# Optimization experiments

Hardware: AMD Instinct MI355X
Metric: run time of the kernel (lower is better)

## Reference

```python
import jax, jax.numpy as jnp
import numpy as np

I, T, L, E, H, W = 256, 256, 32, 128, 7, 7

def setup_inputs() -> dict:
    key = jax.random.key(0)
    k1, k2, k3 = jax.random.split(key, 3)
    image_features = jax.random.normal(k1, (I, E, H, W), dtype=jnp.float32)
    text_features = jax.random.normal(k2, (T, L, E), dtype=jnp.float32)
    text_length = jax.random.randint(k3, (T,), 1, L + 1, dtype=jnp.int32)
    logit_neg_log_temperature = jnp.asarray(-np.log(0.07), dtype=jnp.float32)
    return {
        "image_features": image_features,
        "text_features": text_features,
        "text_length": text_length,
        "logit_neg_log_temperature": logit_neg_log_temperature,
    }

def reference(image_features, text_features, text_length, logit_neg_log_temperature):
    # image_features: [I, E, H, W]; text_features: [T, L, E]
    i, e, h, w = image_features.shape
    img = image_features.reshape(i, e, h * w)            # [I, E, HW]
    # cross-modal similarity per (image, text, token, patch): [I, T, L, HW]
    sim = jnp.einsum('iep,tle->itlp', img, text_features)
    # max over patches, then sum over tokens, normalized by caption length
    match_max = jnp.max(sim, axis=3)                     # [I, T, L]
    match = jnp.sum(match_max, axis=2) / text_length.astype(match_max.dtype)  # [I, T]
    logit_scale = jnp.exp(logit_neg_log_temperature)
    logits_per_image = match * logit_scale
    logits_per_text = match.T * logit_scale
    return (logits_per_image, logits_per_text)
```

## Files before the change

### kernel.cpp

```cpp
#include <hip/hip_runtime.h>
#include <hip/hip_bf16.h>

typedef __attribute__((ext_vector_type(8)))  short bf16x8;
typedef __attribute__((ext_vector_type(16))) float f32x16;

#define I_N 256
#define T_N 256
#define L_N 32
#define E_N 128
#define P_N 49

__global__ __launch_bounds__(256) void pack_all(const float* __restrict__ txt,
                                                const float* __restrict__ img,
                                                unsigned short* __restrict__ bpre,
                                                unsigned short* __restrict__ apre) {
    const int bid = blockIdx.x;
    if (bid < 512) {
        int gid  = bid * 256 + threadIdx.x;
        int lane = gid & 63;
        int ks   = (gid >> 6) & 7;
        int t    = gid >> 9;
        int l    = lane & 31;
        int e0   = ks * 16 + (lane >> 5) * 8;
        const float* src = txt + (t * L_N + l) * E_N + e0;
        union { unsigned short u[8]; bf16x8 v; } o;
        #pragma unroll
        for (int j = 0; j < 8; ++j) {
            __hip_bfloat16 h = __float2bfloat16(src[j]);
            o.u[j] = *reinterpret_cast<unsigned short*>(&h);
        }
        ((bf16x8*)bpre)[gid] = o.v;
    } else {
        int gid   = (bid - 512) * 256 + threadIdx.x;
        int lane  = gid & 63;
        int ks    = (gid >> 6) & 7;
        int pt    = (gid >> 9) & 1;
        int i     = gid >> 10;
        int patch = pt * 32 + (lane & 31);
        int e0    = ks * 16 + (lane >> 5) * 8;
        const float* src = img + i * (E_N * P_N) + e0 * P_N + patch;
        union { unsigned short u[8]; bf16x8 v; } o;
        #pragma unroll
        for (int j = 0; j < 8; ++j) {
            float x = (patch < P_N) ? src[j * P_N] : 0.0f;
            __hip_bfloat16 h = __float2bfloat16(x);
            o.u[j] = *reinterpret_cast<unsigned short*>(&h);
        }
        ((bf16x8*)apre)[gid] = o.v;
    }
}

__global__ __launch_bounds__(256, 3) void clip_mfma(
    const unsigned short* __restrict__ apre,
    const unsigned short* __restrict__ bpre,
    const int*   __restrict__ tlen,
    const float* __restrict__ nlt,
    float*       __restrict__ out) {

    const int wid  = threadIdx.x >> 6;
    const int lane = threadIdx.x & 63;
    const int b    = blockIdx.x;
    const int r    = b % 12;
    const int i    = (b / 12) * 4 + wid;
    const float scale = expf(nlt[0]);
    const bool  lo32  = (lane < 32);

    bf16x8 af[2][8];
    const bf16x8* ap = (const bf16x8*)apre + (size_t)i * 16 * 64;
    #pragma unroll
    for (int pt = 0; pt < 2; ++pt)
        #pragma unroll
        for (int ks = 0; ks < 8; ++ks)
            af[pt][ks] = ap[(pt * 8 + ks) * 64 + lane];

    const bf16x8* bp = (const bf16x8*)bpre;

    #pragma unroll 1
    for (int t = r; t < T_N; t += 12) {
        bf16x8 bf[8];
        const bf16x8* tb = bp + (size_t)t * 8 * 64;
        #pragma unroll
        for (int ks = 0; ks < 8; ++ks)
            bf[ks] = tb[ks * 64 + lane];

        f32x16 a0, a1;
        #pragma unroll
        for (int rr = 0; rr < 16; ++rr) { a0[rr] = 0.0f; a1[rr] = 0.0f; }

        __builtin_amdgcn_s_setprio(1);
        #pragma unroll
        for (int ks = 0; ks < 8; ++ks) {
            a0 = __builtin_amdgcn_mfma_f32_32x32x16_bf16(af[0][ks], bf[ks], a0, 0, 0, 0);
            a1 = __builtin_amdgcn_mfma_f32_32x32x16_bf16(af[1][ks], bf[ks], a1, 0, 0, 0);
        }
        __builtin_amdgcn_s_setprio(0);

        float m = a0[0];
        #pragma unroll
        for (int rr = 1; rr < 16; ++rr) m = fmaxf(m, a0[rr]);
        #pragma unroll
        for (int rr = 0; rr < 8; ++rr)  m = fmaxf(m, a1[rr]);
        m = fmaxf(m, lo32 ? a1[8] : -INFINITY);
        m = fmaxf(m, __shfl_xor(m, 32));
        float s = m;
        #pragma unroll
        for (int off = 1; off <= 16; off <<= 1)
            s += __shfl_xor(s, off);

        if (lane == 0) {
            float match = (s / (float)tlen[t]) * scale;
            out[i * T_N + t]             = match;
            out[I_N * T_N + t * I_N + i] = match;
        }
    }
}

extern "C" void kernel_launch(void* const* d_in, const int* in_sizes, int n_in,
                              void* d_out, int out_size, void* d_ws, size_t ws_size,
                              hipStream_t stream) {
    const float* img  = (const float*)d_in[0];
    const float* txt  = (const float*)d_in[1];
    const int*   tlen = (const int*)d_in[2];
    const float* nlt  = (const float*)d_in[3];
    float*       out  = (float*)d_out;

    unsigned short* bpre = (unsigned short*)d_ws;
    unsigned short* apre = (unsigned short*)((char*)d_ws + (2u << 20));

    pack_all<<<1536, 256, 0, stream>>>(txt, img, bpre, apre);

    clip_mfma<<<768, 256, 0, stream>>>(apre, bpre, tlen, nlt, out);
}
```

Baseline: 47.89 us.

## Double-buffer text tiles in MFMA loop and move token reduction to separate kernel

The MFMA kernel now prefetches the next text tile's B fragments into a second register buffer while it computes the current one, and reduces the per-lane patch maxima with a tree instead of a serial chain. It no longer does the cross-lane token sum and scaling. Instead it writes 64 per-lane maxima per (image, text) pair to workspace, and a new reduce kernel sums them, divides by caption length and writes both outputs. The goal is to hide B-load latency and shorten the dependent chain in the hot loop. In exchange it adds a 16 MB workspace write and read, an extra launch, lower occupancy from the launch bound of 2, and some redundant tiles when the stride does not divide evenly.

Measured after the change: 60.27 us. 25.9% more time.

```diff
diff --git a/kernel.cpp b/kernel.cpp
--- a/kernel.cpp
+++ b/kernel.cpp
@@ -50,20 +50,17 @@
     }
 }
 
-__global__ __launch_bounds__(256, 3) void clip_mfma(
+__global__ __launch_bounds__(256, 2) void clip_mfma(
     const unsigned short* __restrict__ apre,
     const unsigned short* __restrict__ bpre,
-    const int*   __restrict__ tlen,
-    const float* __restrict__ nlt,
-    float*       __restrict__ out) {
+    float* __restrict__ mws) {
 
     const int wid  = threadIdx.x >> 6;
     const int lane = threadIdx.x & 63;
     const int b    = blockIdx.x;
     const int r    = b % 12;
     const int i    = (b / 12) * 4 + wid;
-    const float scale = expf(nlt[0]);
-    const bool  lo32  = (lane < 32);
+    const bool lo32 = (lane < 32);
 
     bf16x8 af[2][8];
     const bf16x8* ap = (const bf16x8*)apre + (size_t)i * 16 * 64;
@@ -75,18 +72,16 @@
 
     const bf16x8* bp = (const bf16x8*)bpre;
 
-    #pragma unroll 1
-    for (int t = r; t < T_N; t += 12) {
-        bf16x8 bf[8];
+    auto loadB = [&](bf16x8 (&bf)[8], int t) {
         const bf16x8* tb = bp + (size_t)t * 8 * 64;
         #pragma unroll
         for (int ks = 0; ks < 8; ++ks)
             bf[ks] = tb[ks * 64 + lane];
+    };
 
-        f32x16 a0, a1;
+    auto mfmaT = [&](f32x16& a0, f32x16& a1, bf16x8 (&bf)[8]) {
         #pragma unroll
         for (int rr = 0; rr < 16; ++rr) { a0[rr] = 0.0f; a1[rr] = 0.0f; }
-
         __builtin_amdgcn_s_setprio(1);
         #pragma unroll
         for (int ks = 0; ks < 8; ++ks) {
@@ -94,24 +89,62 @@
             a1 = __builtin_amdgcn_mfma_f32_32x32x16_bf16(af[1][ks], bf[ks], a1, 0, 0, 0);
         }
         __builtin_amdgcn_s_setprio(0);
+    };
 
-        float m = a0[0];
+    auto treeStore = [&](f32x16& a0, f32x16& a1, int t) {
+        float x[8];
         #pragma unroll
-        for (int rr = 1; rr < 16; ++rr) m = fmaxf(m, a0[rr]);
+        for (int q = 0; q < 8; ++q) x[q] = fmaxf(a0[2 * q], a0[2 * q + 1]);
         #pragma unroll
-        for (int rr = 0; rr < 8; ++rr)  m = fmaxf(m, a1[rr]);
-        m = fmaxf(m, lo32 ? a1[8] : -INFINITY);
-        m = fmaxf(m, __shfl_xor(m, 32));
-        float s = m;
+        for (int q = 0; q < 4; ++q) x[q] = fmaxf(x[q], x[q + 4]);
+        float ma0 = fmaxf(fmaxf(x[0], x[1]), fmaxf(x[2], x[3]));
+        float y[4];
         #pragma unroll
-        for (int off = 1; off <= 16; off <<= 1)
-            s += __shfl_xor(s, off);
+        for (int q = 0; q < 4; ++q) y[q] = fmaxf(a1[2 * q], a1[2 * q + 1]);
+        float ma1 = fmaxf(fmaxf(y[0], y[1]), fmaxf(y[2], y[3]));
+        float m = fmaxf(ma0, ma1);
+        if (lo32) m = fmaxf(m, a1[8]);
+        mws[((size_t)i * T_N + t) * 64 + lane] = m;
+    };
 
-        if (lane == 0) {
-            float match = (s / (float)tlen[t]) * scale;
-            out[i * T_N + t]             = match;
-            out[I_N * T_N + t * I_N + i] = match;
-        }
+    bf16x8 bfA[8], bfB[8];
+    f32x16 aA0, aA1, aB0, aB1;
+
+    loadB(bfA, r);
+    #pragma unroll 1
+    for (int k = 0; k < 22; k += 2) {
+        int t0v = r + 12 * k;
+        int t1v = r + 12 * (k + 1); if (t1v >= T_N) t1v -= 12;
+        loadB(bfB, t1v);
+        mfmaT(aA0, aA1, bfA);
+        treeStore(aA0, aA1, t0v);
+        if (k + 2 < 22) loadB(bfA, r + 12 * (k + 2));
+        mfmaT(aB0, aB1, bfB);
+        treeStore(aB0, aB1, t1v);
+    }
+}
+
+__global__ __launch_bounds__(256) void reduce_k(
+    const float* __restrict__ mws,
+    const int*   __restrict__ tlen,
+    const float* __restrict__ nlt,
+    float*       __restrict__ out) {
+    const int wid  = threadIdx.x >> 6;
+    const int lane = threadIdx.x & 63;
+    const int pair = blockIdx.x * 4 + wid;
+    const int i = pair >> 8, t = pair & 255;
+
+    float v = mws[(size_t)pair * 64 + lane];
+    v = fmaxf(v, __shfl_xor(v, 32));
+    float s = v;
+    #pragma unroll
+    for (int off = 1; off <= 16; off <<= 1)
+        s += __shfl_xor(s, off);
+
+    if (lane == 0) {
+        float match = (s / (float)tlen[t]) * expf(nlt[0]);
+        out[i * T_N + t]             = match;
+        out[I_N * T_N + t * I_N + i] = match;
     }
 }
 
@@ -126,8 +159,9 @@
 
     unsigned short* bpre = (unsigned short*)d_ws;
     unsigned short* apre = (unsigned short*)((char*)d_ws + (2u << 20));
+    float*          mws  = (float*)((char*)d_ws + (6u << 20));
 
     pack_all<<<1536, 256, 0, stream>>>(txt, img, bpre, apre);
-
-    clip_mfma<<<768, 256, 0, stream>>>(apre, bpre, tlen, nlt, out);
+    clip_mfma<<<768, 256, 0, stream>>>(apre, bpre, mws);
+    reduce_k<<<16384, 256, 0, stream>>>(mws, tlen, nlt, out);
 }
```

## Register-block two images per wave and tile text range per block

Applied to the files above, without the earlier changes.

Each wave now keeps A fragments for two images in registers, so every loaded text tile feeds four MFMA chains instead of two. This halves the B-operand global/L2 traffic per MFMA and adds independent accumulators for more instruction-level parallelism. Blocks now cover a contiguous range of 16 texts and 8 images, giving 512 blocks instead of 768, with launch bounds lowered to 2 blocks per CU to make room for the extra registers. The setprio hints are removed. The cost is higher register pressure and lower occupancy, plus a coarser grid.

Result: faster. 45.87 us (-4.2%).

```diff
diff --git a/kernel.cpp b/kernel.cpp
--- a/kernel.cpp
+++ b/kernel.cpp
@@ -50,67 +50,77 @@
     }
 }
 
-__global__ __launch_bounds__(256, 3) void clip_mfma(
+__global__ __launch_bounds__(256, 2) void clip_mfma(
     const unsigned short* __restrict__ apre,
     const unsigned short* __restrict__ bpre,
     const int*   __restrict__ tlen,
     const float* __restrict__ nlt,
     float*       __restrict__ out) {
 
-    const int wid  = threadIdx.x >> 6;
-    const int lane = threadIdx.x & 63;
-    const int b    = blockIdx.x;
-    const int r    = b % 12;
-    const int i    = (b / 12) * 4 + wid;
+    const int wid   = threadIdx.x >> 6;
+    const int lane  = threadIdx.x & 63;
+    const int b     = blockIdx.x;
+    const int tbase = (b >> 5) << 4;
+    const int i0    = (b & 31) * 8 + wid * 2;
     const float scale = expf(nlt[0]);
     const bool  lo32  = (lane < 32);
 
-    bf16x8 af[2][8];
-    const bf16x8* ap = (const bf16x8*)apre + (size_t)i * 16 * 64;
+    bf16x8 af[2][2][8];
     #pragma unroll
-    for (int pt = 0; pt < 2; ++pt)
+    for (int im = 0; im < 2; ++im) {
+        const bf16x8* ap = (const bf16x8*)apre + (size_t)(i0 + im) * 16 * 64;
         #pragma unroll
-        for (int ks = 0; ks < 8; ++ks)
-            af[pt][ks] = ap[(pt * 8 + ks) * 64 + lane];
+        for (int pt = 0; pt < 2; ++pt)
+            #pragma unroll
+            for (int ks = 0; ks < 8; ++ks)
+                af[im][pt][ks] = ap[(pt * 8 + ks) * 64 + lane];
+    }
 
     const bf16x8* bp = (const bf16x8*)bpre;
 
     #pragma unroll 1
-    for (int t = r; t < T_N; t += 12) {
+    for (int t = tbase; t < tbase + 16; ++t) {
         bf16x8 bf[8];
         const bf16x8* tb = bp + (size_t)t * 8 * 64;
         #pragma unroll
         for (int ks = 0; ks < 8; ++ks)
             bf[ks] = tb[ks * 64 + lane];
 
-        f32x16 a0, a1;
+        f32x16 a00, a01, a10, a11;
         #pragma unroll
-        for (int rr = 0; rr < 16; ++rr) { a0[rr] = 0.0f; a1[rr] = 0.0f; }
+        for (int rr = 0; rr < 16; ++rr) {
+            a00[rr] = 0.0f; a01[rr] = 0.0f; a10[rr] = 0.0f; a11[rr] = 0.0f;
+        }
 
-        __builtin_amdgcn_s_setprio(1);
         #pragma unroll
         for (int ks = 0; ks < 8; ++ks) {
-            a0 = __builtin_amdgcn_mfma_f32_32x32x16_bf16(af[0][ks], bf[ks], a0, 0, 0, 0);
-            a1 = __builtin_amdgcn_mfma_f32_32x32x16_bf16(af[1][ks], bf[ks], a1, 0, 0, 0);
+            a00 = __builtin_amdgcn_mfma_f32_32x32x16_bf16(af[0][0][ks], bf[ks], a00, 0, 0, 0);
+            a01 = __builtin_amdgcn_mfma_f32_32x32x16_bf16(af[0][1][ks], bf[ks], a01, 0, 0, 0);
+            a10 = __builtin_amdgcn_mfma_f32_32x32x16_bf16(af[1][0][ks], bf[ks], a10, 0, 0, 0);
+            a11 = __builtin_amdgcn_mfma_f32_32x32x16_bf16(af[1][1][ks], bf[ks], a11, 0, 0, 0);
         }
-        __builtin_amdgcn_s_setprio(0);
 
-        float m = a0[0];
         #pragma unroll
-        for (int rr = 1; rr < 16; ++rr) m = fmaxf(m, a0[rr]);
-        #pragma unroll
-        for (int rr = 0; rr < 8; ++rr)  m = fmaxf(m, a1[rr]);
-        m = fmaxf(m, lo32 ? a1[8] : -INFINITY);
-        m = fmaxf(m, __shfl_xor(m, 32));
-        float s = m;
-        #pragma unroll
-        for (int off = 1; off <= 16; off <<= 1)
-            s += __shfl_xor(s, off);
-
-        if (lane == 0) {
-            float match = (s / (float)tlen[t]) * scale;
-            out[i * T_N + t]             = match;
-            out[I_N * T_N + t * I_N + i] = match;
+        for (int im = 0; im < 2; ++im) {
+            const f32x16& c0 = im ? a10 : a00;
+            const f32x16& c1 = im ? a11 : a01;
+            float m = c0[0];
+            #pragma unroll
+            for (int rr = 1; rr < 16; ++rr) m = fmaxf(m, c0[rr]);
+            #pragma unroll
+            for (int rr = 0; rr < 8; ++rr)  m = fmaxf(m, c1[rr]);
+            m = fmaxf(m, lo32 ? c1[8] : -INFINITY);
+            m = fmaxf(m, __shfl_xor(m, 32));
+            float s = m;
+            #pragma unroll
+            for (int off = 1; off <= 16; off <<= 1)
+                s += __shfl_xor(s, off);
+            if (lane == 0) {
+                float match = (s / (float)tlen[t]) * scale;
+                const int i = i0 + im;
+                out[i * T_N + t]             = match;
+                out[I_N * T_N + t * I_N + i] = match;
+            }
         }
     }
 }
@@ -128,6 +138,5 @@
     unsigned short* apre = (unsigned short*)((char*)d_ws + (2u << 20));
 
     pack_all<<<1536, 256, 0, stream>>>(txt, img, bpre, apre);
-
-    clip_mfma<<<768, 256, 0, stream>>>(apre, bpre, tlen, nlt, out);
+    clip_mfma<<<512, 256, 0, stream>>>(apre, bpre, tlen, nlt, out);
 }
```

## Double-buffer text tiles with register prefetch and rebalance grid to 512 blocks

Applied to the files above, without the earlier changes.

The MFMA kernel now gives each block a contiguous run of 32 texts instead of a stride-12 set, and launches 512 blocks instead of 768. It keeps two register buffers of B fragments so the load for the next text is issued while the current one's MFMAs and max/sum reduction run. The occupancy hint drops from 3 to 2 blocks per SIMD group to make room for the extra registers. The s_setprio hints are removed. The trade-off is lower occupancy and fewer blocks, in exchange for explicit latency hiding and even work per block (32 texts each versus uneven 21/22).

Result: slower. 53.23 us (+11.2%).

```diff
diff --git a/kernel.cpp b/kernel.cpp
--- a/kernel.cpp
+++ b/kernel.cpp
@@ -50,7 +50,7 @@
     }
 }
 
-__global__ __launch_bounds__(256, 3) void clip_mfma(
+__global__ __launch_bounds__(256, 2) void clip_mfma(
     const unsigned short* __restrict__ apre,
     const unsigned short* __restrict__ bpre,
     const int*   __restrict__ tlen,
@@ -60,8 +60,8 @@
     const int wid  = threadIdx.x >> 6;
     const int lane = threadIdx.x & 63;
     const int b    = blockIdx.x;
-    const int r    = b % 12;
-    const int i    = (b / 12) * 4 + wid;
+    const int t0   = (b & 7) * 32;
+    const int i    = (b >> 3) * 4 + wid;
     const float scale = expf(nlt[0]);
     const bool  lo32  = (lane < 32);
 
@@ -75,43 +75,56 @@
 
     const bf16x8* bp = (const bf16x8*)bpre;
 
-    #pragma unroll 1
-    for (int t = r; t < T_N; t += 12) {
-        bf16x8 bf[8];
+    auto loadB = [&](bf16x8 (&bf)[8], int t) {
         const bf16x8* tb = bp + (size_t)t * 8 * 64;
         #pragma unroll
         for (int ks = 0; ks < 8; ++ks)
             bf[ks] = tb[ks * 64 + lane];
+    };
 
-        f32x16 a0, a1;
+    auto mfmaT = [&](f32x16& a0, f32x16& a1, bf16x8 (&bf)[8]) {
         #pragma unroll
         for (int rr = 0; rr < 16; ++rr) { a0[rr] = 0.0f; a1[rr] = 0.0f; }
-
-        __builtin_amdgcn_s_setprio(1);
         #pragma unroll
         for (int ks = 0; ks < 8; ++ks) {
             a0 = __builtin_amdgcn_mfma_f32_32x32x16_bf16(af[0][ks], bf[ks], a0, 0, 0, 0);
             a1 = __builtin_amdgcn_mfma_f32_32x32x16_bf16(af[1][ks], bf[ks], a1, 0, 0, 0);
         }
-        __builtin_amdgcn_s_setprio(0);
+    };
 
-        float m = a0[0];
+    auto reduceT = [&](f32x16& c0, f32x16& c1, int t) {
+        float m = c0[0];
         #pragma unroll
-        for (int rr = 1; rr < 16; ++rr) m = fmaxf(m, a0[rr]);
+        for (int rr = 1; rr < 16; ++rr) m = fmaxf(m, c0[rr]);
         #pragma unroll
-        for (int rr = 0; rr < 8; ++rr)  m = fmaxf(m, a1[rr]);
-        m = fmaxf(m, lo32 ? a1[8] : -INFINITY);
+        for (int rr = 0; rr < 8; ++rr)  m = fmaxf(m, c1[rr]);
+        m = fmaxf(m, lo32 ? c1[8] : -INFINITY);
         m = fmaxf(m, __shfl_xor(m, 32));
         float s = m;
         #pragma unroll
         for (int off = 1; off <= 16; off <<= 1)
             s += __shfl_xor(s, off);
-
         if (lane == 0) {
             float match = (s / (float)tlen[t]) * scale;
             out[i * T_N + t]             = match;
             out[I_N * T_N + t * I_N + i] = match;
         }
+    };
+
+    bf16x8 bfA[8], bfB[8];
+    f32x16 aA0, aA1, aB0, aB1;
+
+    loadB(bfA, t0);
+    loadB(bfB, t0 + 1);
+
+    #pragma unroll 1
+    for (int k = 0; k < 32; k += 2) {
+        mfmaT(aA0, aA1, bfA);
+        if (k + 2 < 32) loadB(bfA, t0 + k + 2);
+        reduceT(aA0, aA1, t0 + k);
+        mfmaT(aB0, aB1, bfB);
+        if (k + 3 < 32) loadB(bfB, t0 + k + 3);
+        reduceT(aB0, aB1, t0 + k + 1);
     }
 }
 
@@ -128,6 +141,5 @@
     unsigned short* apre = (unsigned short*)((char*)d_ws + (2u << 20));
 
     pack_all<<<1536, 256, 0, stream>>>(txt, img, bpre, apre);
-
-    clip_mfma<<<768, 256, 0, stream>>>(apre, bpre, tlen, nlt, out);
+    clip_mfma<<<512, 256, 0, stream>>>(apre, bpre, tlen, nlt, out);
 }
```
